# Kernel tuning notes

Hardware: AMD Instinct MI355X
Metric: run time of the kernel (lower is better)

The kernel has to match this reference:

```python
import jax, jax.numpy as jnp
import numpy as np

N, B, T, H, DF, OD, AUX = 325, 128, 12, 128, 32, 2, 2
IN_DIM = OD + AUX


def setup_inputs() -> dict:
    key = jax.random.key(0)
    ks = jax.random.split(key, 20)

    def nrm(k, shape, fan):
        return jax.random.normal(k, shape, dtype=jnp.float32) * (fan ** -0.5)

    def adj(k):
        a = jax.random.uniform(k, (N, N), dtype=jnp.float32)
        return a / jnp.sum(a, axis=1, keepdims=True)  # row-normalized adjacency

    feature = jax.random.normal(ks[0], (N, DF), dtype=jnp.float32)
    label = jax.random.normal(ks[1], (N, B, T, OD + AUX), dtype=jnp.float32)
    state0 = jax.random.normal(ks[2], (N, B, H), dtype=jnp.float32)
    state1 = jax.random.normal(ks[3], (N, B, H), dtype=jnp.float32)
    Wx0 = nrm(ks[4], (IN_DIM + DF, 3 * H), IN_DIM + DF)
    Wh0 = nrm(ks[5], (H, 3 * H), H)
    b0 = jnp.zeros((3 * H,), jnp.float32)
    Wx1 = nrm(ks[6], (H + DF, 3 * H), H + DF)
    Wh1 = nrm(ks[7], (H, 3 * H), H)
    b1 = jnp.zeros((3 * H,), jnp.float32)
    A01, A02, A11, A12 = adj(ks[8]), adj(ks[9]), adj(ks[10]), adj(ks[11])
    Wg01 = nrm(ks[12], (H, H), H)
    Wg02 = nrm(ks[13], (H, H), H)
    Wg11 = nrm(ks[14], (H, H), H)
    Wg12 = nrm(ks[15], (H, H), H)
    Wp = nrm(ks[16], (H + DF, OD), H + DF)
    bp = jnp.zeros((OD,), jnp.float32)
    return dict(feature=feature, label=label, state0=state0, state1=state1,
                Wx0=Wx0, Wh0=Wh0, b0=b0, Wx1=Wx1, Wh1=Wh1, b1=b1,
                A01=A01, A02=A02, Wg01=Wg01, Wg02=Wg02,
                A11=A11, A12=A12, Wg11=Wg11, Wg12=Wg12,
                Wp=Wp, bp=bp, is_training=0)


def reference(feature, label, state0, state1, Wx0, Wh0, b0, Wx1, Wh1, b1,
              A01, A02, Wg01, Wg02, A11, A12, Wg11, Wg12, Wp, bp, is_training):
    n, b, t, _ = label.shape
    od = Wp.shape[1]
    h = Wh0.shape[0]
    aux = label[..., od:]                              # [n,b,t,aux]
    feat_b = jnp.broadcast_to(feature[:, None, :], (n, b, feature.shape[-1]))

    def gru(x_data, hs, Wx, Wh, bias):
        # cell.forward_single: input = [data, node meta-feature]
        x = jnp.concatenate([x_data, feat_b], axis=-1)
        g = x @ Wx + bias                              # [n,b,3h]
        hW = hs @ Wh
        z = jax.nn.sigmoid(g[..., :h] + hW[..., :h])
        r = jax.nn.sigmoid(g[..., h:2 * h] + hW[..., h:2 * h])
        c = jnp.tanh(g[..., 2 * h:] + r * hW[..., 2 * h:])
        return z * hs + (1.0 - z) * c

    def gconv(d, A1, W1, A2, W2):
        # sum of graph convs, averaged over the graphs of this layer
        m1 = jnp.einsum('nm,mbh->nbh', A1, d) @ W1
        m2 = jnp.einsum('nm,mbh->nbh', A2, d) @ W2
        return 0.5 * (m1 + m2)

    aux_t = jnp.moveaxis(aux, 2, 0)                    # [t,n,b,aux]
    aux_prev = jnp.concatenate([jnp.zeros_like(aux_t[:1]), aux_t[:-1]], axis=0)
    first = jnp.arange(t) == 0

    def step(carry, xs):
        h0, h1, prev = carry
        a_prev, is_first = xs
        # i==0: data = go (zeros); else data = concat(prev_output, aux[i-1])
        data = jnp.where(is_first, 0.0,
                         jnp.concatenate([prev, a_prev], axis=-1))
        h0n = gru(data, h0, Wx0, Wh0, b0)
        d = gconv(h0n, A01, Wg01, A02, Wg02)
        h1n = gru(d, h1, Wx1, Wh1, b1)
        d = gconv(h1n, A11, Wg11, A12, Wg12)
        out = jnp.concatenate([d, feat_b], axis=-1) @ Wp + bp  # proj
        return (h0n, h1n, out), out

    init = (state0, state1, jnp.zeros((n, b, od), label.dtype))
    _, outs = jax.lax.scan(step, init, (aux_prev, first))
    return jnp.moveaxis(outs, 0, 2)                    # [n,b,t,od]
```

## Files before the change

kernel.cpp:

```cpp
#include <hip/hip_runtime.h>
#include <math.h>

#define NN 325
#define NPAD 352
#define KPAD 352
#define BBv 128
#define TTv 12
#define HHv 128
#define DFDv 32
#define ODDv 2
#define G3v 384
#define GX 11
#define GY 64

typedef __attribute__((ext_vector_type(8))) short bf16x8;
typedef __attribute__((ext_vector_type(4))) float f32x4;
typedef __attribute__((ext_vector_type(8))) unsigned short ushort8;
typedef unsigned short ushort;

__device__ __forceinline__ ushort f2bf(float f) {
    union { float f; unsigned u; } v; v.f = f;
    unsigned r = v.u + 0x7FFFu + ((v.u >> 16) & 1u);
    return (ushort)(r >> 16);
}
__device__ __forceinline__ float bf2f(ushort u) {
    union { unsigned u; float f; } v; v.u = ((unsigned)u) << 16; return v.f;
}
__device__ __forceinline__ float sigmoidf_(float x) { return 1.0f / (1.0f + __expf(-x)); }

#define MFMA(a,b,c) __builtin_amdgcn_mfma_f32_16x16x32_bf16((a),(b),(c),0,0,0)

__global__ void wtrans_kernel(const float* __restrict__ W, ushort* __restrict__ Wt,
                              int K, int N, int KP) {
    int idx = blockIdx.x * 256 + threadIdx.x;
    if (idx >= N * KP) return;
    int n = idx / KP, k = idx - n * KP;
    Wt[idx] = f2bf(k < K ? W[(size_t)k * N + n] : 0.f);
}
__global__ void aconv_kernel(const float* __restrict__ A, ushort* __restrict__ Ab) {
    int idx = blockIdx.x * 256 + threadIdx.x;
    if (idx >= NPAD * KPAD) return;
    int n = idx / KPAD, m = idx - n * KPAD;
    Ab[idx] = f2bf((n < NN && m < NN) ? A[n * NN + m] : 0.f);
}
__global__ void strans_kernel(const float* __restrict__ S, ushort* __restrict__ xt) {
    int idx = blockIdx.x * 256 + threadIdx.x;
    if (idx >= BBv * HHv * KPAD) return;
    int col = idx / KPAD, n = idx - col * KPAD;
    int b = col >> 7, ch = col & 127;
    xt[idx] = (n < NN) ? f2bf(S[((size_t)n * BBv + b) * HHv + ch]) : (ushort)0;
}
__global__ void gxf_kernel(const float* __restrict__ W, const float* __restrict__ bias,
                           const float* __restrict__ feat, float* __restrict__ gxf, int row0) {
    int n = blockIdx.x, j = threadIdx.x;
    int nc = (n < NN) ? n : NN - 1;
    float a = bias[j];
    #pragma unroll 8
    for (int k = 0; k < DFDv; ++k) a = fmaf(feat[nc * DFDv + k], W[(size_t)(row0 + k) * G3v + j], a);
    gxf[(size_t)n * G3v + j] = a;
}
__global__ void pfeat_kernel(const float* __restrict__ Wp, const float* __restrict__ bp,
                             const float* __restrict__ feat, float* __restrict__ pf) {
    int n = blockIdx.x, c = threadIdx.x;
    if (c >= 2) return;
    int nc = (n < NN) ? n : NN - 1;
    float a = bp[c];
    #pragma unroll 8
    for (int k = 0; k < DFDv; ++k) a = fmaf(feat[nc * DFDv + k], Wp[(size_t)(HHv + k) * ODDv + c], a);
    pf[n * 2 + c] = a;
}

__global__ __launch_bounds__(512) void gru0_init(
    const float* __restrict__ state0,
    const float* __restrict__ gxf0,
    const ushort* __restrict__ Wht,
    ushort* __restrict__ xt)
{
    __shared__ ushort hs[32][136];
    __shared__ ushort hnb[32][136];
    const int n0 = blockIdx.x * 32;
    const int b  = blockIdx.y;
    const int tid = threadIdx.x;
    {
        int i = tid >> 4, c0 = (tid & 15) * 8;
        int n = n0 + i; if (n > NN - 1) n = NN - 1;
        const float* src = state0 + ((size_t)(n * BBv + b) * HHv + c0);
        float4 v0 = *(const float4*)src;
        float4 v1 = *(const float4*)(src + 4);
        ushort* dst = &hs[i][c0];
        dst[0]=f2bf(v0.x); dst[1]=f2bf(v0.y); dst[2]=f2bf(v0.z); dst[3]=f2bf(v0.w);
        dst[4]=f2bf(v1.x); dst[5]=f2bf(v1.y); dst[6]=f2bf(v1.z); dst[7]=f2bf(v1.w);
    }
    __syncthreads();

    const int w = tid >> 6, l = tid & 63, lr = l & 15, lk = l >> 4;
    const int ch = w * 16 + lr;

    f32x4 az[2], ar[2], agc[2], ahc[2];
    #pragma unroll
    for (int rt = 0; rt < 2; ++rt)
        #pragma unroll
        for (int i = 0; i < 4; ++i) {
            int nl = rt * 16 + lk * 4 + i;
            const float* g = gxf0 + (size_t)(n0 + nl) * G3v;
            az[rt][i]  = g[ch];
            ar[rt][i]  = g[128 + ch];
            agc[rt][i] = g[256 + ch];
            ahc[rt][i] = 0.f;
        }
    #pragma unroll
    for (int kk = 0; kk < 4; ++kk) {
        const int kb = kk * 32 + lk * 8;
        bf16x8 bz = *(const bf16x8*)(Wht + (size_t)(ch) * HHv + kb);
        bf16x8 br = *(const bf16x8*)(Wht + (size_t)(128 + ch) * HHv + kb);
        bf16x8 bc = *(const bf16x8*)(Wht + (size_t)(256 + ch) * HHv + kb);
        #pragma unroll
        for (int rt = 0; rt < 2; ++rt) {
            bf16x8 a = *(const bf16x8*)&hs[rt * 16 + lr][kb];
            az[rt] = MFMA(a, bz, az[rt]);
            ar[rt] = MFMA(a, br, ar[rt]);
            ahc[rt] = MFMA(a, bc, ahc[rt]);
        }
    }
    #pragma unroll
    for (int rt = 0; rt < 2; ++rt)
        #pragma unroll
        for (int i = 0; i < 4; ++i) {
            int r2 = rt * 16 + lk * 4 + i;
            float z  = sigmoidf_(az[rt][i]);
            float rr = sigmoidf_(ar[rt][i]);
            float c  = tanhf(agc[rt][i] + rr * ahc[rt][i]);
            float hn = z * bf2f(hs[r2][ch]) + (1.f - z) * c;
            hnb[r2][ch] = f2bf(hn);
        }
    __syncthreads();
    {
        int chx = tid >> 2, g = tid & 3;
        ushort8 v;
        #pragma unroll
        for (int k = 0; k < 8; ++k) v[k] = hnb[g * 8 + k][chx];
        *(ushort8*)(xt + (size_t)(b * HHv + chx) * KPAD + n0 + g * 8) = v;
    }
}

template<int WHICH>
__global__ __launch_bounds__(512) void fused_step(
    const ushort* __restrict__ xtB,
    const ushort* __restrict__ xtH,
    ushort* __restrict__ xtO,
    const ushort* __restrict__ Ab1,
    const ushort* __restrict__ Ab2,
    const ushort* __restrict__ W1t,
    const ushort* __restrict__ W2t,
    const ushort* __restrict__ Wxt,
    const ushort* __restrict__ Wht,
    const float* __restrict__ gxf,
    const float* __restrict__ label,
    const float* __restrict__ Wp,
    const float* __restrict__ pfeat,
    float* __restrict__ out,
    int t)
{
    constexpr int KXP = (WHICH == 0) ? 128 : 32;
    __shared__ ushort m1s[64][136];
    __shared__ ushort m2s[64][136];
    __shared__ ushort hs[64][136];
    __shared__ ushort xs[64][40];
    __shared__ float  os[64][2];

    int rid = blockIdx.x + GX * blockIdx.y;
    int xcd = rid & 7, rank = rid >> 3;
    int qy = rank / GX;
    const int n0 = (rank - qy * GX) * 32;
    const int b0 = (xcd * 8 + qy) * 2;

    const int tid = threadIdx.x;
    const int w = tid >> 6, l = tid & 63, lr = l & 15, lk = l >> 4;

    {
        int chg = tid >> 1, g = tid & 1;
        int bl = chg >> 7, ch = chg & 127;
        const ushort* src = xtH + (size_t)((b0 + bl) * HHv + ch) * KPAD + n0 + g * 16;
        ushort8 v0 = *(const ushort8*)src;
        ushort8 v1 = *(const ushort8*)(src + 8);
        #pragma unroll
        for (int k = 0; k < 8; ++k) hs[bl * 32 + g * 16 + k][ch] = v0[k];
        #pragma unroll
        for (int k = 0; k < 8; ++k) hs[bl * 32 + g * 16 + 8 + k][ch] = v1[k];
    }

    f32x4 m1[2][2], m2[2][2];
    #pragma unroll
    for (int rt = 0; rt < 2; ++rt)
        #pragma unroll
        for (int f = 0; f < 2; ++f) {
            m1[rt][f] = (f32x4){0.f,0.f,0.f,0.f};
            m2[rt][f] = (f32x4){0.f,0.f,0.f,0.f};
        }
    #pragma unroll 2
    for (int kk = 0; kk < KPAD / 32; ++kk) {
        const int kb = kk * 32 + lk * 8;
        bf16x8 a1[2], a2[2];
        #pragma unroll
        for (int rt = 0; rt < 2; ++rt) {
            a1[rt] = *(const bf16x8*)(Ab1 + (size_t)(n0 + rt * 16 + lr) * KPAD + kb);
            a2[rt] = *(const bf16x8*)(Ab2 + (size_t)(n0 + rt * 16 + lr) * KPAD + kb);
        }
        #pragma unroll
        for (int f = 0; f < 2; ++f) {
            bf16x8 bx = *(const bf16x8*)(xtB + (size_t)(b0 * HHv + w * 32 + f * 16 + lr) * KPAD + kb);
            #pragma unroll
            for (int rt = 0; rt < 2; ++rt) {
                m1[rt][f] = MFMA(a1[rt], bx, m1[rt][f]);
                m2[rt][f] = MFMA(a2[rt], bx, m2[rt][f]);
            }
        }
    }
    #pragma unroll
    for (int rt = 0; rt < 2; ++rt)
        #pragma unroll
        for (int f = 0; f < 2; ++f) {
            int colg = w * 32 + f * 16 + lr;
            int bl = colg >> 7, ch = colg & 127;
            #pragma unroll
            for (int i = 0; i < 4; ++i) {
                int r2 = bl * 32 + rt * 16 + lk * 4 + i;
                m1s[r2][ch] = f2bf(m1[rt][f][i]);
                m2s[r2][ch] = f2bf(m2[rt][f][i]);
            }
        }
    __syncthreads();

    f32x4 dacc[4];
    #pragma unroll
    for (int rt = 0; rt < 4; ++rt) dacc[rt] = (f32x4){0.f,0.f,0.f,0.f};
    #pragma unroll
    for (int kk = 0; kk < 4; ++kk) {
        const int kb = kk * 32 + lk * 8;
        bf16x8 b1 = *(const bf16x8*)(W1t + (size_t)(w * 16 + lr) * HHv + kb);
        bf16x8 b2 = *(const bf16x8*)(W2t + (size_t)(w * 16 + lr) * HHv + kb);
        #pragma unroll
        for (int rt = 0; rt < 4; ++rt) {
            bf16x8 a1x = *(const bf16x8*)&m1s[rt * 16 + lr][kb];
            bf16x8 a2x = *(const bf16x8*)&m2s[rt * 16 + lr][kb];
            dacc[rt] = MFMA(a1x, b1, dacc[rt]);
            dacc[rt] = MFMA(a2x, b2, dacc[rt]);
        }
    }
    __syncthreads();

    {
        const int ch = w * 16 + lr;
        #pragma unroll
        for (int rt = 0; rt < 4; ++rt)
            #pragma unroll
            for (int i = 0; i < 4; ++i)
                m1s[rt * 16 + lk * 4 + i][ch] = f2bf(0.5f * dacc[rt][i]);
    }
    __syncthreads();

    if (WHICH == 1) {
        {
            int r2p = tid >> 3, sub = tid & 7;
            float a0 = 0.f, a1 = 0.f;
            #pragma unroll
            for (int q = 0; q < 16; ++q) {
                int k = sub * 16 + q;
                float v = bf2f(m1s[r2p][k]);
                a0 = fmaf(v, Wp[k * 2 + 0], a0);
                a1 = fmaf(v, Wp[k * 2 + 1], a1);
            }
            #pragma unroll
            for (int o = 4; o > 0; o >>= 1) {
                a0 += __shfl_down(a0, o, 8);
                a1 += __shfl_down(a1, o, 8);
            }
            if (sub == 0) {
                int n = n0 + (r2p & 31);
                os[r2p][0] = a0 + pfeat[n * 2 + 0];
                os[r2p][1] = a1 + pfeat[n * 2 + 1];
            }
        }
        __syncthreads();
        if (tid < 128) {
            int r2 = tid >> 1, c = tid & 1;
            int n = n0 + (r2 & 31), b = b0 + (r2 >> 5);
            if (n < NN)
                out[(((size_t)n * BBv + b) * TTv + t) * ODDv + c] = os[r2][c];
        }
        for (int e = tid; e < 64 * 32; e += 512) {
            int r2 = e >> 5, k = e & 31;
            int n = n0 + (r2 & 31), b = b0 + (r2 >> 5);
            int nc = (n > NN - 1) ? NN - 1 : n;
            ushort v;
            if (k < 2)      v = f2bf(os[r2][k]);
            else if (k < 4) v = f2bf(label[(((size_t)nc * BBv + b) * TTv + t) * 4 + 2 + (k - 2)]);
            else            v = 0;
            xs[r2][k] = v;
        }
        __syncthreads();
    }

    const int ch = w * 16 + lr;
    f32x4 az[4], ar[4], agc[4], ahc[4];
    #pragma unroll
    for (int rt = 0; rt < 4; ++rt)
        #pragma unroll
        for (int i = 0; i < 4; ++i) {
            int nl = (rt * 16 + lk * 4 + i) & 31;
            const float* g = gxf + (size_t)(n0 + nl) * G3v;
            az[rt][i]  = g[ch];
            ar[rt][i]  = g[128 + ch];
            agc[rt][i] = g[256 + ch];
            ahc[rt][i] = 0.f;
        }
    #pragma unroll
    for (int kk = 0; kk < KXP / 32; ++kk) {
        const int kb = kk * 32 + lk * 8;
        bf16x8 bz = *(const bf16x8*)(Wxt + (size_t)ch * KXP + kb);
        bf16x8 br = *(const bf16x8*)(Wxt + (size_t)(128 + ch) * KXP + kb);
        bf16x8 bc = *(const bf16x8*)(Wxt + (size_t)(256 + ch) * KXP + kb);
        #pragma unroll
        for (int rt = 0; rt < 4; ++rt) {
            bf16x8 a = (WHICH == 0)
                ? *(const bf16x8*)&m1s[rt * 16 + lr][kb]
                : *(const bf16x8*)&xs[rt * 16 + lr][kb];
            az[rt] = MFMA(a, bz, az[rt]);
            ar[rt] = MFMA(a, br, ar[rt]);
            agc[rt] = MFMA(a, bc, agc[rt]);
        }
    }
    #pragma unroll
    for (int kk = 0; kk < 4; ++kk) {
        const int kb = kk * 32 + lk * 8;
        bf16x8 bz = *(const bf16x8*)(Wht + (size_t)ch * HHv + kb);
        bf16x8 br = *(const bf16x8*)(Wht + (size_t)(128 + ch) * HHv + kb);
        bf16x8 bc = *(const bf16x8*)(Wht + (size_t)(256 + ch) * HHv + kb);
        #pragma unroll
        for (int rt = 0; rt < 4; ++rt) {
            bf16x8 a = *(const bf16x8*)&hs[rt * 16 + lr][kb];
            az[rt] = MFMA(a, bz, az[rt]);
            ar[rt] = MFMA(a, br, ar[rt]);
            ahc[rt] = MFMA(a, bc, ahc[rt]);
        }
    }

    #pragma unroll
    for (int rt = 0; rt < 4; ++rt)
        #pragma unroll
        for (int i = 0; i < 4; ++i) {
            int r2 = rt * 16 + lk * 4 + i;
            float z  = sigmoidf_(az[rt][i]);
            float rr = sigmoidf_(ar[rt][i]);
            float c  = tanhf(agc[rt][i] + rr * ahc[rt][i]);
            float hn = z * bf2f(hs[r2][ch]) + (1.f - z) * c;
            m2s[r2][ch] = f2bf(hn);
        }
    __syncthreads();

    {
        int chg = tid >> 1, g = tid & 1;
        int bl = chg >> 7, chx = chg & 127;
        ushort8 v0, v1;
        #pragma unroll
        for (int k = 0; k < 8; ++k) v0[k] = m2s[bl * 32 + g * 16 + k][chx];
        #pragma unroll
        for (int k = 0; k < 8; ++k) v1[k] = m2s[bl * 32 + g * 16 + 8 + k][chx];
        ushort* dst = xtO + (size_t)((b0 + bl) * HHv + chx) * KPAD + n0 + g * 16;
        *(ushort8*)dst = v0;
        *(ushort8*)(dst + 8) = v1;
    }
}

extern "C" void kernel_launch(void* const* d_in, const int* in_sizes, int n_in,
                              void* d_out, int out_size, void* d_ws, size_t ws_size,
                              hipStream_t stream)
{
    const float* feature = (const float*)d_in[0];
    const float* label   = (const float*)d_in[1];
    const float* state0  = (const float*)d_in[2];
    const float* state1  = (const float*)d_in[3];
    const float* Wx0 = (const float*)d_in[4];
    const float* Wh0 = (const float*)d_in[5];
    const float* b0  = (const float*)d_in[6];
    const float* Wx1 = (const float*)d_in[7];
    const float* Wh1 = (const float*)d_in[8];
    const float* b1  = (const float*)d_in[9];
    const float* A01 = (const float*)d_in[10];
    const float* A02 = (const float*)d_in[11];
    const float* Wg01 = (const float*)d_in[12];
    const float* Wg02 = (const float*)d_in[13];
    const float* A11 = (const float*)d_in[14];
    const float* A12 = (const float*)d_in[15];
    const float* Wg11 = (const float*)d_in[16];
    const float* Wg12 = (const float*)d_in[17];
    const float* Wp  = (const float*)d_in[18];
    const float* bp  = (const float*)d_in[19];

    float* out = (float*)d_out;

    char* p = (char*)d_ws;
    auto alloc = [&](size_t bytes) {
        void* r = (void*)p; p += (bytes + 255) & ~(size_t)255; return r;
    };
    const size_t XTSZ = (size_t)BBv * HHv * KPAD;
    ushort* xt0[2] = { (ushort*)alloc(XTSZ * 2), (ushort*)alloc(XTSZ * 2) };
    ushort* xt1[2] = { (ushort*)alloc(XTSZ * 2), (ushort*)alloc(XTSZ * 2) };
    ushort* Ab01 = (ushort*)alloc((size_t)NPAD * KPAD * 2);
    ushort* Ab02 = (ushort*)alloc((size_t)NPAD * KPAD * 2);
    ushort* Ab11 = (ushort*)alloc((size_t)NPAD * KPAD * 2);
    ushort* Ab12 = (ushort*)alloc((size_t)NPAD * KPAD * 2);
    ushort* Wx0t = (ushort*)alloc((size_t)G3v * 32 * 2);
    ushort* Wh0t = (ushort*)alloc((size_t)G3v * HHv * 2);
    ushort* Wx1t = (ushort*)alloc((size_t)G3v * HHv * 2);
    ushort* Wh1t = (ushort*)alloc((size_t)G3v * HHv * 2);
    ushort* Wg01t = (ushort*)alloc((size_t)HHv * HHv * 2);
    ushort* Wg02t = (ushort*)alloc((size_t)HHv * HHv * 2);
    ushort* Wg11t = (ushort*)alloc((size_t)HHv * HHv * 2);
    ushort* Wg12t = (ushort*)alloc((size_t)HHv * HHv * 2);
    float*  gxf0 = (float*)alloc((size_t)NPAD * G3v * 4);
    float*  gxf1 = (float*)alloc((size_t)NPAD * G3v * 4);
    float*  pfe  = (float*)alloc((size_t)NPAD * 2 * 4);

    auto cdiv = [](int a, int b) { return (a + b - 1) / b; };
    wtrans_kernel<<<cdiv(G3v * 32, 256), 256, 0, stream>>>(Wx0, Wx0t, 4, G3v, 32);
    wtrans_kernel<<<cdiv(G3v * HHv, 256), 256, 0, stream>>>(Wh0, Wh0t, HHv, G3v, HHv);
    wtrans_kernel<<<cdiv(G3v * HHv, 256), 256, 0, stream>>>(Wx1, Wx1t, HHv, G3v, HHv);
    wtrans_kernel<<<cdiv(G3v * HHv, 256), 256, 0, stream>>>(Wh1, Wh1t, HHv, G3v, HHv);
    wtrans_kernel<<<cdiv(HHv * HHv, 256), 256, 0, stream>>>(Wg01, Wg01t, HHv, HHv, HHv);
    wtrans_kernel<<<cdiv(HHv * HHv, 256), 256, 0, stream>>>(Wg02, Wg02t, HHv, HHv, HHv);
    wtrans_kernel<<<cdiv(HHv * HHv, 256), 256, 0, stream>>>(Wg11, Wg11t, HHv, HHv, HHv);
    wtrans_kernel<<<cdiv(HHv * HHv, 256), 256, 0, stream>>>(Wg12, Wg12t, HHv, HHv, HHv);
    aconv_kernel<<<cdiv(NPAD * KPAD, 256), 256, 0, stream>>>(A01, Ab01);
    aconv_kernel<<<cdiv(NPAD * KPAD, 256), 256, 0, stream>>>(A02, Ab02);
    aconv_kernel<<<cdiv(NPAD * KPAD, 256), 256, 0, stream>>>(A11, Ab11);
    aconv_kernel<<<cdiv(NPAD * KPAD, 256), 256, 0, stream>>>(A12, Ab12);
    gxf_kernel<<<NPAD, G3v, 0, stream>>>(Wx0, b0, feature, gxf0, 4);
    gxf_kernel<<<NPAD, G3v, 0, stream>>>(Wx1, b1, feature, gxf1, 128);
    pfeat_kernel<<<NPAD, 64, 0, stream>>>(Wp, bp, feature, pfe);
    strans_kernel<<<cdiv((int)XTSZ, 256), 256, 0, stream>>>(state1, xt1[0]);

    gru0_init<<<dim3(GX, BBv), 512, 0, stream>>>(state0, gxf0, Wh0t, xt0[0]);

    const dim3 grid(GX, GY);
    for (int t = 0; t < TTv; ++t) {
        fused_step<0><<<grid, 512, 0, stream>>>(
            xt0[t & 1], xt1[t & 1], xt1[(t + 1) & 1],
            Ab01, Ab02, Wg01t, Wg02t, Wx1t, Wh1t, gxf1,
            nullptr, nullptr, nullptr, nullptr, t);
        fused_step<1><<<grid, 512, 0, stream>>>(
            xt1[(t + 1) & 1], xt0[t & 1], xt0[(t + 1) & 1],
            Ab11, Ab12, Wg11t, Wg12t, Wx0t, Wh0t, gxf0,
            label, Wp, pfe, out, t);
    }
}
```

Before: 1.810 ms.

## Fold node-feature input projection into GRU MFMA and reuse shared buffers

The precomputed per-node feature projection (gxf) is replaced by extending the GRU input GEMM's K dimension with the bf16 node features, so the feature contribution is computed by extra MFMAs inside the fused step. Bias is added per channel at activation time instead. The xs/os shared arrays are aliased into the m1s/m2s buffers to cut LDS use, with launch_bounds raised to request higher occupancy. This trades a gathered fp32 gxf load per element for extra MFMA work and an added barrier, and moves the feature term to bf16 precision.

```diff
diff --git a/kernel.cpp b/kernel.cpp
--- a/kernel.cpp
+++ b/kernel.cpp
@@ -37,11 +37,24 @@
     int n = idx / KP, k = idx - n * KP;
     Wt[idx] = f2bf(k < K ? W[(size_t)k * N + n] : 0.f);
 }
+__global__ void wtransx0_kernel(const float* __restrict__ W, ushort* __restrict__ Wt) {
+    int idx = blockIdx.x * 256 + threadIdx.x;
+    if (idx >= G3v * 64) return;
+    int n = idx / 64, k = idx - n * 64;
+    int src = (k < 32) ? (4 + k) : ((k < 36) ? (k - 32) : -1);
+    Wt[idx] = f2bf(src >= 0 ? W[(size_t)src * G3v + n] : 0.f);
+}
 __global__ void aconv_kernel(const float* __restrict__ A, ushort* __restrict__ Ab) {
     int idx = blockIdx.x * 256 + threadIdx.x;
     if (idx >= NPAD * KPAD) return;
     int n = idx / KPAD, m = idx - n * KPAD;
     Ab[idx] = f2bf((n < NN && m < NN) ? A[n * NN + m] : 0.f);
+}
+__global__ void fconv_kernel(const float* __restrict__ F, ushort* __restrict__ Fb) {
+    int idx = blockIdx.x * 256 + threadIdx.x;
+    if (idx >= NPAD * DFDv) return;
+    int n = idx >> 5, c = idx & 31;
+    Fb[idx] = f2bf(n < NN ? F[n * DFDv + c] : 0.f);
 }
 __global__ void strans_kernel(const float* __restrict__ S, ushort* __restrict__ xt) {
     int idx = blockIdx.x * 256 + threadIdx.x;
@@ -144,7 +157,7 @@
 }
 
 template<int WHICH>
-__global__ __launch_bounds__(512) void fused_step(
+__global__ __launch_bounds__(512, 6) void fused_step(
     const ushort* __restrict__ xtB,
     const ushort* __restrict__ xtH,
     ushort* __restrict__ xtO,
@@ -154,19 +167,19 @@
     const ushort* __restrict__ W2t,
     const ushort* __restrict__ Wxt,
     const ushort* __restrict__ Wht,
-    const float* __restrict__ gxf,
+    const float* __restrict__ bias,
+    const ushort* __restrict__ featb,
     const float* __restrict__ label,
     const float* __restrict__ Wp,
     const float* __restrict__ pfeat,
     float* __restrict__ out,
     int t)
 {
-    constexpr int KXP = (WHICH == 0) ? 128 : 32;
+    constexpr int KXP = (WHICH == 0) ? 160 : 64;
     __shared__ ushort m1s[64][136];
     __shared__ ushort m2s[64][136];
     __shared__ ushort hs[64][136];
-    __shared__ ushort xs[64][40];
-    __shared__ float  os[64][2];
+    __shared__ ushort fs[32][32];
 
     int rid = blockIdx.x + GX * blockIdx.y;
     int xcd = rid & 7, rank = rid >> 3;
@@ -187,6 +200,10 @@
         for (int k = 0; k < 8; ++k) hs[bl * 32 + g * 16 + k][ch] = v0[k];
         #pragma unroll
         for (int k = 0; k < 8; ++k) hs[bl * 32 + g * 16 + 8 + k][ch] = v1[k];
+    }
+    if (tid < 128) {
+        int nl = tid >> 2, c0 = (tid & 3) * 8;
+        *(ushort8*)&fs[nl][c0] = *(const ushort8*)(featb + (n0 + nl) * DFDv + c0);
     }
 
     f32x4 m1[2][2], m2[2][2];
@@ -277,8 +294,9 @@
             }
             if (sub == 0) {
                 int n = n0 + (r2p & 31);
-                os[r2p][0] = a0 + pfeat[n * 2 + 0];
-                os[r2p][1] = a1 + pfeat[n * 2 + 1];
+                float* os = (float*)&m1s[r2p][128];
+                os[0] = a0 + pfeat[n * 2 + 0];
+                os[1] = a1 + pfeat[n * 2 + 1];
             }
         }
         __syncthreads();
@@ -286,34 +304,32 @@
             int r2 = tid >> 1, c = tid & 1;
             int n = n0 + (r2 & 31), b = b0 + (r2 >> 5);
             if (n < NN)
-                out[(((size_t)n * BBv + b) * TTv + t) * ODDv + c] = os[r2][c];
+                out[(((size_t)n * BBv + b) * TTv + t) * ODDv + c] =
+                    ((const float*)&m1s[r2][128])[c];
         }
         for (int e = tid; e < 64 * 32; e += 512) {
             int r2 = e >> 5, k = e & 31;
             int n = n0 + (r2 & 31), b = b0 + (r2 >> 5);
             int nc = (n > NN - 1) ? NN - 1 : n;
             ushort v;
-            if (k < 2)      v = f2bf(os[r2][k]);
+            if (k < 2)      v = f2bf(((const float*)&m1s[r2][128])[k]);
             else if (k < 4) v = f2bf(label[(((size_t)nc * BBv + b) * TTv + t) * 4 + 2 + (k - 2)]);
             else            v = 0;
-            xs[r2][k] = v;
+            m2s[r2][k] = v;
         }
         __syncthreads();
     }
 
     const int ch = w * 16 + lr;
+    const float bzv = bias[ch], brv = bias[128 + ch], bcv = bias[256 + ch];
     f32x4 az[4], ar[4], agc[4], ahc[4];
     #pragma unroll
-    for (int rt = 0; rt < 4; ++rt)
-        #pragma unroll
-        for (int i = 0; i < 4; ++i) {
-            int nl = (rt * 16 + lk * 4 + i) & 31;
-            const float* g = gxf + (size_t)(n0 + nl) * G3v;
-            az[rt][i]  = g[ch];
-            ar[rt][i]  = g[128 + ch];
-            agc[rt][i] = g[256 + ch];
-            ahc[rt][i] = 0.f;
-        }
+    for (int rt = 0; rt < 4; ++rt) {
+        az[rt] = (f32x4){0.f,0.f,0.f,0.f};
+        ar[rt] = (f32x4){0.f,0.f,0.f,0.f};
+        agc[rt] = (f32x4){0.f,0.f,0.f,0.f};
+        ahc[rt] = (f32x4){0.f,0.f,0.f,0.f};
+    }
     #pragma unroll
     for (int kk = 0; kk < KXP / 32; ++kk) {
         const int kb = kk * 32 + lk * 8;
@@ -322,9 +338,14 @@
         bf16x8 bc = *(const bf16x8*)(Wxt + (size_t)(256 + ch) * KXP + kb);
         #pragma unroll
         for (int rt = 0; rt < 4; ++rt) {
-            bf16x8 a = (WHICH == 0)
-                ? *(const bf16x8*)&m1s[rt * 16 + lr][kb]
-                : *(const bf16x8*)&xs[rt * 16 + lr][kb];
+            bf16x8 a;
+            if (WHICH == 0) {
+                if (kk < 4) a = *(const bf16x8*)&m1s[rt * 16 + lr][kb];
+                else        a = *(const bf16x8*)&fs[(rt & 1) * 16 + lr][lk * 8];
+            } else {
+                if (kk == 0) a = *(const bf16x8*)&fs[(rt & 1) * 16 + lr][lk * 8];
+                else         a = *(const bf16x8*)&m2s[rt * 16 + lr][lk * 8];
+            }
             az[rt] = MFMA(a, bz, az[rt]);
             ar[rt] = MFMA(a, br, ar[rt]);
             agc[rt] = MFMA(a, bc, agc[rt]);
@@ -345,14 +366,16 @@
         }
     }
 
+    if (WHICH == 1) __syncthreads();
+
     #pragma unroll
     for (int rt = 0; rt < 4; ++rt)
         #pragma unroll
         for (int i = 0; i < 4; ++i) {
             int r2 = rt * 16 + lk * 4 + i;
-            float z  = sigmoidf_(az[rt][i]);
-            float rr = sigmoidf_(ar[rt][i]);
-            float c  = tanhf(agc[rt][i] + rr * ahc[rt][i]);
+            float z  = sigmoidf_(az[rt][i] + bzv);
+            float rr = sigmoidf_(ar[rt][i] + brv);
+            float c  = tanhf(agc[rt][i] + bcv + rr * ahc[rt][i]);
             float hn = z * bf2f(hs[r2][ch]) + (1.f - z) * c;
             m2s[r2][ch] = f2bf(hn);
         }
@@ -410,22 +433,22 @@
     ushort* Ab02 = (ushort*)alloc((size_t)NPAD * KPAD * 2);
     ushort* Ab11 = (ushort*)alloc((size_t)NPAD * KPAD * 2);
     ushort* Ab12 = (ushort*)alloc((size_t)NPAD * KPAD * 2);
-    ushort* Wx0t = (ushort*)alloc((size_t)G3v * 32 * 2);
+    ushort* Wx0t = (ushort*)alloc((size_t)G3v * 64 * 2);
     ushort* Wh0t = (ushort*)alloc((size_t)G3v * HHv * 2);
-    ushort* Wx1t = (ushort*)alloc((size_t)G3v * HHv * 2);
+    ushort* Wx1t = (ushort*)alloc((size_t)G3v * 160 * 2);
     ushort* Wh1t = (ushort*)alloc((size_t)G3v * HHv * 2);
     ushort* Wg01t = (ushort*)alloc((size_t)HHv * HHv * 2);
     ushort* Wg02t = (ushort*)alloc((size_t)HHv * HHv * 2);
     ushort* Wg11t = (ushort*)alloc((size_t)HHv * HHv * 2);
     ushort* Wg12t = (ushort*)alloc((size_t)HHv * HHv * 2);
+    ushort* featb = (ushort*)alloc((size_t)NPAD * DFDv * 2);
     float*  gxf0 = (float*)alloc((size_t)NPAD * G3v * 4);
-    float*  gxf1 = (float*)alloc((size_t)NPAD * G3v * 4);
     float*  pfe  = (float*)alloc((size_t)NPAD * 2 * 4);
 
     auto cdiv = [](int a, int b) { return (a + b - 1) / b; };
-    wtrans_kernel<<<cdiv(G3v * 32, 256), 256, 0, stream>>>(Wx0, Wx0t, 4, G3v, 32);
+    wtransx0_kernel<<<cdiv(G3v * 64, 256), 256, 0, stream>>>(Wx0, Wx0t);
     wtrans_kernel<<<cdiv(G3v * HHv, 256), 256, 0, stream>>>(Wh0, Wh0t, HHv, G3v, HHv);
-    wtrans_kernel<<<cdiv(G3v * HHv, 256), 256, 0, stream>>>(Wx1, Wx1t, HHv, G3v, HHv);
+    wtrans_kernel<<<cdiv(G3v * 160, 256), 256, 0, stream>>>(Wx1, Wx1t, 160, G3v, 160);
     wtrans_kernel<<<cdiv(G3v * HHv, 256), 256, 0, stream>>>(Wh1, Wh1t, HHv, G3v, HHv);
     wtrans_kernel<<<cdiv(HHv * HHv, 256), 256, 0, stream>>>(Wg01, Wg01t, HHv, HHv, HHv);
     wtrans_kernel<<<cdiv(HHv * HHv, 256), 256, 0, stream>>>(Wg02, Wg02t, HHv, HHv, HHv);
@@ -435,8 +458,8 @@
     aconv_kernel<<<cdiv(NPAD * KPAD, 256), 256, 0, stream>>>(A02, Ab02);
     aconv_kernel<<<cdiv(NPAD * KPAD, 256), 256, 0, stream>>>(A11, Ab11);
     aconv_kernel<<<cdiv(NPAD * KPAD, 256), 256, 0, stream>>>(A12, Ab12);
+    fconv_kernel<<<cdiv(NPAD * DFDv, 256), 256, 0, stream>>>(feature, featb);
     gxf_kernel<<<NPAD, G3v, 0, stream>>>(Wx0, b0, feature, gxf0, 4);
-    gxf_kernel<<<NPAD, G3v, 0, stream>>>(Wx1, b1, feature, gxf1, 128);
     pfeat_kernel<<<NPAD, 64, 0, stream>>>(Wp, bp, feature, pfe);
     strans_kernel<<<cdiv((int)XTSZ, 256), 256, 0, stream>>>(state1, xt1[0]);
 
@@ -446,11 +469,11 @@
     for (int t = 0; t < TTv; ++t) {
         fused_step<0><<<grid, 512, 0, stream>>>(
             xt0[t & 1], xt1[t & 1], xt1[(t + 1) & 1],
-            Ab01, Ab02, Wg01t, Wg02t, Wx1t, Wh1t, gxf1,
+            Ab01, Ab02, Wg01t, Wg02t, Wx1t, Wh1t, b1, featb,
             nullptr, nullptr, nullptr, nullptr, t);
         fused_step<1><<<grid, 512, 0, stream>>>(
             xt1[(t + 1) & 1], xt0[t & 1], xt0[(t + 1) & 1],
-            Ab11, Ab12, Wg11t, Wg12t, Wx0t, Wh0t, gxf0,
+            Ab11, Ab12, Wg11t, Wg12t, Wx0t, Wh0t, b0, featb,
             label, Wp, pfe, out, t);
     }
 }
```

Measured after the change: 1.833 ms. Within noise of the previous version (+1.2%).
